# Kernel tuning notes

Hardware: AMD Instinct MI355X
Metric: run time of the kernel (lower is better)

## Reference

```python
import jax, jax.numpy as jnp
import numpy as np
import math

WS = 8
N = WS * WS
DIM = 384
HEADS = 12

def _rel_buffers():
    coords = np.stack(np.meshgrid(np.arange(WS), np.arange(WS), indexing='ij')).reshape(2, -1)
    rel = (coords[:, :, None] - coords[:, None, :]).transpose(1, 2, 0)  # [n,n,2]
    table = rel.astype(np.float32) / (WS - 1) * 8.0
    table = np.sign(table) * np.log2(np.abs(table) + 1.0) / np.log2(8.0)
    idx = rel.copy()
    idx[..., 0] += WS - 1
    idx[..., 1] += WS - 1
    idx[..., 0] *= 2 * WS - 1
    index = idx.sum(-1).astype(np.int32)  # [n,n] in [0, 225)
    return jnp.asarray(table), jnp.asarray(index)

def setup_inputs() -> dict:
    key = jax.random.key(0)
    ks = jax.random.split(key, 9)
    b_ = 4096
    nW = 1024
    table, index = _rel_buffers()
    return {
        'x': jax.random.normal(ks[0], (b_, N, DIM), jnp.float32),
        'mask': jax.random.normal(ks[1], (nW, N, N), jnp.float32),
        'qkv_w': jax.random.normal(ks[2], (DIM, 3 * DIM), jnp.float32) * 0.02,
        'qkv_b': jax.random.normal(ks[3], (3 * DIM,), jnp.float32) * 0.02,
        'proj_w': jax.random.normal(ks[4], (DIM, DIM), jnp.float32) * 0.02,
        'proj_b': jax.random.normal(ks[5], (DIM,), jnp.float32) * 0.02,
        'logit_scale': jnp.full((HEADS, 1, 1), math.log(10.0), jnp.float32),
        'cpb_w1': jax.random.normal(ks[6], (2, 512), jnp.float32) * 0.5,
        'cpb_b1': jax.random.normal(ks[7], (512,), jnp.float32) * 0.02,
        'cpb_w2': jax.random.normal(ks[8], (512, HEADS), jnp.float32) * 0.05,
        'rel_coords_table': table,
        'rel_pos_index': index,
    }

def _l2norm(t):
    # torch F.normalize: x / max(||x||, eps)
    return t / jnp.maximum(jnp.linalg.norm(t, axis=-1, keepdims=True), 1e-12)

def reference(x, mask, qkv_w, qkv_b, proj_w, proj_b, logit_scale, cpb_w1, cpb_b1, cpb_w2, rel_coords_table, rel_pos_index):
    b_, n, c = x.shape
    h = HEADS
    d = c // h
    qkv = (x @ qkv_w + qkv_b).reshape(b_, n, 3, h, d).transpose(2, 0, 3, 1, 4)
    q, k, v = qkv[0], qkv[1], qkv[2]  # [b,h,n,d]
    q = _l2norm(q)
    k = _l2norm(k)
    scale = jnp.exp(jnp.minimum(logit_scale, math.log(100.0)))  # [h,1,1]
    attn = jnp.einsum('bhqd,bhkd->bhqk', q, k) * scale[None]
    # continuous position bias MLP + gather
    bias_tab = jax.nn.relu(rel_coords_table @ cpb_w1 + cpb_b1) @ cpb_w2  # [n,n,h]
    bias = bias_tab.reshape(-1, h)[rel_pos_index.reshape(-1)].reshape(n, n, h)
    bias = 16.0 * jax.nn.sigmoid(bias.transpose(2, 0, 1))  # [h,n,n]
    attn = attn + bias[None]
    nW = mask.shape[0]
    attn = attn.reshape(b_ // nW, nW, h, n, n) + mask[None, :, None]
    attn = attn.reshape(b_, h, n, n)
    attn = jax.nn.softmax(attn, axis=-1)
    out = jnp.einsum('bhqk,bhkd->bqhd', attn, v).reshape(b_, n, c)
    return out @ proj_w + proj_b
```

## Files before the change

kernel.cpp:

```cpp
#include <hip/hip_runtime.h>
#include <hip/hip_fp16.h>

typedef _Float16 f16;
typedef _Float16 f16x8 __attribute__((ext_vector_type(8)));
typedef _Float16 f16x4 __attribute__((ext_vector_type(4)));
typedef float f32x4 __attribute__((ext_vector_type(4)));

#define NH 12
#define NWIN 4096

__device__ __forceinline__ void gload16(const void* g, void* l) {
  __builtin_amdgcn_global_load_lds(
      (const __attribute__((address_space(1))) void*)g,
      (__attribute__((address_space(3))) void*)l, 16, 0, 0);
}


__global__ __launch_bounds__(256) void k_cvt_x(const float* __restrict__ in,
                                               f16* __restrict__ out, long n4) {
  long i = (long)blockIdx.x * 256 + threadIdx.x;
  long stride = (long)gridDim.x * 256;
  for (; i < n4; i += stride) {
    float4 v = ((const float4*)in)[i];
    f16x4 o = {(f16)v.x, (f16)v.y, (f16)v.z, (f16)v.w};
    ((f16x4*)out)[i] = o;
  }
}

__global__ __launch_bounds__(256) void k_transpose(const float* __restrict__ in,
                                                   f16* __restrict__ out, int K, int N) {
  long i = (long)blockIdx.x * 256 + threadIdx.x;
  if (i >= (long)K * N) return;
  int n = (int)(i / K);
  int k = (int)(i - (long)n * K);
  out[i] = (f16)in[(long)k * N + n];
}

__global__ __launch_bounds__(64) void k_cpb(const float* __restrict__ table,
                                            const int* __restrict__ ridx,
                                            const float* __restrict__ w1,
                                            const float* __restrict__ b1,
                                            const float* __restrict__ w2,
                                            float* __restrict__ biasout) {
  int p = blockIdx.x * 64 + threadIdx.x;
  int idx = ridx[p];
  float t0 = table[idx * 2], t1 = table[idx * 2 + 1];
  float acc[NH] = {};
  for (int u = 0; u < 512; u++) {
    float hv = fmaxf(t0 * w1[u] + t1 * w1[512 + u] + b1[u], 0.f);
#pragma unroll
    for (int h = 0; h < NH; h++) acc[h] += hv * w2[u * NH + h];
  }
  for (int h = 0; h < NH; h++) biasout[h * 4096 + p] = 16.f / (1.f + __expf(-acc[h]));
}

template <int MODE, int NXB>
__global__ __launch_bounds__(256) void k_gemm(const f16* __restrict__ A,
                                              const f16* __restrict__ Bt,
                                              const float* __restrict__ bias,
                                              void* __restrict__ out, int K) {
  __shared__ f16 As[128 * 32];
  __shared__ f16 Bs[128 * 32];
  const int lin = blockIdx.x;
  const int idx = lin % (NXB * 8);
  const int xn = idx >> 3;
  const int ym = (lin / (NXB * 8)) * 8 + (idx & 7);
  const int tid = threadIdx.x;
  const int lane = tid & 63, wid = tid >> 6;
  const int wm = wid & 1, wn = wid >> 1;

  f32x4 acc[4][4] = {};
  const long arow = (long)ym * 128;
  const long brow = (long)xn * 128;

  for (int kk = 0; kk < K; kk += 32) {
    __syncthreads();
#pragma unroll
    for (int j = 0; j < 2; j++) {
      int r = wid * 32 + j * 16 + (lane >> 2);
      int co = kk + (lane & 3) * 8;
      gload16(A + (arow + r) * K + co, As + (wid * 32 + j * 16) * 32);
      gload16(Bt + (brow + r) * K + co, Bs + (wid * 32 + j * 16) * 32);
    }
    __syncthreads();
    f16x8 am[4], bn[4];
#pragma unroll
    for (int t = 0; t < 4; t++) {
      am[t] = *(const f16x8*)&As[(wm * 64 + t * 16 + (lane & 15)) * 32 + (lane >> 4) * 8];
      bn[t] = *(const f16x8*)&Bs[(wn * 64 + t * 16 + (lane & 15)) * 32 + (lane >> 4) * 8];
    }
#pragma unroll
    for (int mt = 0; mt < 4; mt++)
#pragma unroll
      for (int nt = 0; nt < 4; nt++)
        acc[mt][nt] = __builtin_amdgcn_mfma_f32_16x16x32_f16(am[mt], bn[nt], acc[mt][nt], 0, 0, 0);
  }

  const int quad = lane >> 4, col0 = lane & 15;
#pragma unroll
  for (int mt = 0; mt < 4; mt++) {
#pragma unroll
    for (int nt = 0; nt < 4; nt++) {
      int c = xn * 128 + wn * 64 + nt * 16 + col0;
      float bc = bias[c];
#pragma unroll
      for (int reg = 0; reg < 4; reg++) {
        long m = arow + wm * 64 + mt * 16 + quad * 4 + reg;
        float v = acc[mt][nt][reg] + bc;
        if (MODE == 0) {
          int which = c / 384;
          int rem = c - which * 384;
          int hh = rem >> 5, d = rem & 31;
          long b = m >> 6;
          long n = m & 63;
          ((f16*)out)[(((long)which * (NWIN * NH) + b * NH + hh) * 64 + n) * 32 + d] = (f16)v;
        } else {
          ((float*)out)[m * 384 + c] = v;
        }
      }
    }
  }
}

__global__ __launch_bounds__(256) void k_attn(const f16* __restrict__ qkv,
                                              const float* __restrict__ mask,
                                              const float* __restrict__ bias,
                                              const float* __restrict__ lsc,
                                              f16* __restrict__ aout) {
  __shared__ f16 qs[64 * 32];
  __shared__ f16 ks[64 * 32];
  __shared__ f16 vt[32 * 72];
  __shared__ float sm[64 * 64];
  __shared__ f16 ps[64 * 72];

  const int bh = blockIdx.x;
  const int b = bh / NH;
  const int h = bh - b * NH;
  const int w = b & 1023;
  const int tid = threadIdx.x;
  const int lane = tid & 63, wid = tid >> 6;

  const long HB = (long)NWIN * NH * 64 * 32;
  const f16* qg = qkv + (long)bh * 2048;

  f16x8 qv = ((const f16x8*)qg)[tid];
  f16x8 kv = ((const f16x8*)(qg + HB))[tid];
  f16x8 vv = ((const f16x8*)(qg + 2 * HB))[tid];

  float ssq = 0.f, ssk = 0.f;
#pragma unroll
  for (int j = 0; j < 8; j++) {
    float xq = (float)qv[j]; ssq += xq * xq;
    float xk = (float)kv[j]; ssk += xk * xk;
  }
  ssq += __shfl_xor(ssq, 1); ssq += __shfl_xor(ssq, 2);
  ssk += __shfl_xor(ssk, 1); ssk += __shfl_xor(ssk, 2);
  float lscale = __expf(fminf(lsc[h], 4.6051701860f));
  float qsc = lscale / fmaxf(sqrtf(ssq), 1e-12f);
  float ksc = 1.f / fmaxf(sqrtf(ssk), 1e-12f);

  f16x8 qn, kn;
#pragma unroll
  for (int j = 0; j < 8; j++) {
    qn[j] = (f16)((float)qv[j] * qsc);
    kn[j] = (f16)((float)kv[j] * ksc);
  }
  ((f16x8*)qs)[tid] = qn;
  ((f16x8*)ks)[tid] = kn;
  {
    int vrow = tid >> 2, d0 = (tid & 3) * 8;
#pragma unroll
    for (int j = 0; j < 8; j++) vt[(d0 + j) * 72 + vrow] = vv[j];
  }
  {
    const float4* bp = (const float4*)(bias + (long)h * 4096);
    const float4* mp = (const float4*)(mask + (long)w * 4096);
#pragma unroll
    for (int j = 0; j < 4; j++) {
      int i4 = tid + 256 * j;
      float4 bb = bp[i4];
      float4 mm = mp[i4];
      bb.x += mm.x; bb.y += mm.y; bb.z += mm.z; bb.w += mm.w;
      ((float4*)sm)[i4] = bb;
    }
  }
  __syncthreads();

  const int col0 = lane & 15, quad = lane >> 4;
  f16x8 aq = *(const f16x8*)&qs[(wid * 16 + col0) * 32 + quad * 8];
  f32x4 s[4];
#pragma unroll
  for (int nt = 0; nt < 4; nt++) {
    f16x8 bk = *(const f16x8*)&ks[(nt * 16 + col0) * 32 + quad * 8];
    f32x4 z = {};
    s[nt] = __builtin_amdgcn_mfma_f32_16x16x32_f16(aq, bk, z, 0, 0, 0);
  }

  float rinv[4];
#pragma unroll
  for (int reg = 0; reg < 4; reg++) {
    int r = wid * 16 + quad * 4 + reg;
    float m_ = -1e30f;
#pragma unroll
    for (int nt = 0; nt < 4; nt++) {
      s[nt][reg] += sm[r * 64 + nt * 16 + col0];
      m_ = fmaxf(m_, s[nt][reg]);
    }
    m_ = fmaxf(m_, __shfl_xor(m_, 1));
    m_ = fmaxf(m_, __shfl_xor(m_, 2));
    m_ = fmaxf(m_, __shfl_xor(m_, 4));
    m_ = fmaxf(m_, __shfl_xor(m_, 8));
    float l_ = 0.f;
#pragma unroll
    for (int nt = 0; nt < 4; nt++) {
      float p = __expf(s[nt][reg] - m_);
      s[nt][reg] = p;
      l_ += p;
    }
    l_ += __shfl_xor(l_, 1);
    l_ += __shfl_xor(l_, 2);
    l_ += __shfl_xor(l_, 4);
    l_ += __shfl_xor(l_, 8);
    rinv[reg] = 1.f / l_;
#pragma unroll
    for (int nt = 0; nt < 4; nt++) ps[r * 72 + nt * 16 + col0] = (f16)s[nt][reg];
  }
  __syncthreads();

  f32x4 o[2] = {};
#pragma unroll
  for (int kkk = 0; kkk < 2; kkk++) {
    f16x8 ap = *(const f16x8*)&ps[(wid * 16 + col0) * 72 + kkk * 32 + quad * 8];
#pragma unroll
    for (int nt = 0; nt < 2; nt++) {
      f16x8 bv = *(const f16x8*)&vt[(nt * 16 + col0) * 72 + kkk * 32 + quad * 8];
      o[nt] = __builtin_amdgcn_mfma_f32_16x16x32_f16(ap, bv, o[nt], 0, 0, 0);
    }
  }
#pragma unroll
  for (int nt = 0; nt < 2; nt++)
#pragma unroll
    for (int reg = 0; reg < 4; reg++) {
      int r = wid * 16 + quad * 4 + reg;
      int d = nt * 16 + col0;
      float v = o[nt][reg] * rinv[reg];
      aout[((long)b * 64 + r) * 384 + h * 32 + d] = (f16)v;
    }
}


extern "C" void kernel_launch(void* const* d_in, const int* in_sizes, int n_in,
                              void* d_out, int out_size, void* d_ws, size_t ws_size,
                              hipStream_t stream) {
  const float* x      = (const float*)d_in[0];
  const float* mask   = (const float*)d_in[1];
  const float* qkv_w  = (const float*)d_in[2];
  const float* qkv_b  = (const float*)d_in[3];
  const float* proj_w = (const float*)d_in[4];
  const float* proj_b = (const float*)d_in[5];
  const float* lsc    = (const float*)d_in[6];
  const float* cpb_w1 = (const float*)d_in[7];
  const float* cpb_b1 = (const float*)d_in[8];
  const float* cpb_w2 = (const float*)d_in[9];
  const float* table  = (const float*)d_in[10];
  const int* ridx     = (const int*)d_in[11];
  float* out = (float*)d_out;

  char* ws = (char*)d_ws;
  const long NQKV = (long)3 * NWIN * NH * 64 * 32;
  f16* qkvbuf = (f16*)ws;
  f16* xh     = (f16*)(ws + NQKV * 2);
  f16* aoutbuf = xh;
  f16* wtq    = (f16*)(ws + NQKV * 2 + 201326592L);
  f16* wtp    = (f16*)(ws + NQKV * 2 + 201326592L + 884736L);
  float* biasbuf = (float*)(ws + NQKV * 2 + 201326592L + 884736L + 294912L);

  k_cvt_x<<<4096, 256, 0, stream>>>(x, xh, 100663296L / 4);
  k_transpose<<<(1152 * 384) / 256, 256, 0, stream>>>(qkv_w, wtq, 384, 1152);
  k_transpose<<<(384 * 384) / 256, 256, 0, stream>>>(proj_w, wtp, 384, 384);
  k_cpb<<<64, 64, 0, stream>>>(table, ridx, cpb_w1, cpb_b1, cpb_w2, biasbuf);

  k_gemm<0, 9><<<2048 * 9, 256, 0, stream>>>(xh, wtq, qkv_b, qkvbuf, 384);

  k_attn<<<NWIN * NH, 256, 0, stream>>>(qkvbuf, mask, biasbuf, lsc, aoutbuf);

  k_gemm<1, 3><<<2048 * 3, 256, 0, stream>>>(aoutbuf, wtp, proj_b, out, 384);
}
```

Baseline: 1.536 ms.

## Make GEMM persistent with double-buffered LDS prefetch across tiles

Turns the GEMM kernel into a persistent one. Each block now walks a run of consecutive output tiles (24 for QKV, 8 for projection) on a fixed grid of 768 blocks. Shared memory is double-buffered so the next K-slice, or the first slice of the next tile, is fetched with global_load_lds while the current slice feeds the MFMAs. This cuts one barrier per K step and hides load latency. In exchange the grouped-M swizzle used for L2 reuse is dropped in favour of row-major tile order, and the larger LDS footprint plus the 3-blocks-per-SM launch bound may constrain occupancy.

```diff
diff --git a/kernel.cpp b/kernel.cpp
--- a/kernel.cpp
+++ b/kernel.cpp
@@ -54,68 +54,104 @@
   for (int h = 0; h < NH; h++) biasout[h * 4096 + p] = 16.f / (1.f + __expf(-acc[h]));
 }
 
-template <int MODE, int NXB>
-__global__ __launch_bounds__(256) void k_gemm(const f16* __restrict__ A,
-                                              const f16* __restrict__ Bt,
-                                              const float* __restrict__ bias,
-                                              void* __restrict__ out, int K) {
-  __shared__ f16 As[128 * 32];
-  __shared__ f16 Bs[128 * 32];
-  const int lin = blockIdx.x;
-  const int idx = lin % (NXB * 8);
-  const int xn = idx >> 3;
-  const int ym = (lin / (NXB * 8)) * 8 + (idx & 7);
+template <int MODE, int NXB, int TPB>
+__global__ __launch_bounds__(256, 3) void k_gemm(const f16* __restrict__ A,
+                                                 const f16* __restrict__ Bt,
+                                                 const float* __restrict__ bias,
+                                                 void* __restrict__ out, int K) {
+  __shared__ f16 smem[2 * 8192];
   const int tid = threadIdx.x;
   const int lane = tid & 63, wid = tid >> 6;
   const int wm = wid & 1, wn = wid >> 1;
+  const int quad = lane >> 4, col0 = lane & 15;
+
+  const int r0 = wid * 32 + (lane >> 2);
+  const int co0 = (lane & 3) * 8;
+  const int ldsoff = (wid * 32) * 32;
+
+  const int lin0 = blockIdx.x * TPB;
+
+  auto rows_of = [&](int t, long& ar, long& br) {
+    int lin = lin0 + t;
+    int ym = lin / NXB;
+    int xn = lin - ym * NXB;
+    ar = (long)ym * 128;
+    br = (long)xn * 128;
+  };
+
+  auto stage = [&](int buf, long ar, long br, int kk) {
+#pragma unroll
+    for (int j = 0; j < 2; j++) {
+      gload16(A + (ar + r0 + j * 16) * K + co0 + kk,
+              smem + buf * 8192 + ldsoff + j * 16 * 32);
+      gload16(Bt + (br + r0 + j * 16) * K + co0 + kk,
+              smem + buf * 8192 + 4096 + ldsoff + j * 16 * 32);
+    }
+  };
 
   f32x4 acc[4][4] = {};
-  const long arow = (long)ym * 128;
-  const long brow = (long)xn * 128;
-
-  for (int kk = 0; kk < K; kk += 32) {
-    __syncthreads();
-#pragma unroll
-    for (int j = 0; j < 2; j++) {
-      int r = wid * 32 + j * 16 + (lane >> 2);
-      int co = kk + (lane & 3) * 8;
-      gload16(A + (arow + r) * K + co, As + (wid * 32 + j * 16) * 32);
-      gload16(Bt + (brow + r) * K + co, Bs + (wid * 32 + j * 16) * 32);
-    }
-    __syncthreads();
-    f16x8 am[4], bn[4];
-#pragma unroll
-    for (int t = 0; t < 4; t++) {
-      am[t] = *(const f16x8*)&As[(wm * 64 + t * 16 + (lane & 15)) * 32 + (lane >> 4) * 8];
-      bn[t] = *(const f16x8*)&Bs[(wn * 64 + t * 16 + (lane & 15)) * 32 + (lane >> 4) * 8];
-    }
-#pragma unroll
-    for (int mt = 0; mt < 4; mt++)
-#pragma unroll
-      for (int nt = 0; nt < 4; nt++)
-        acc[mt][nt] = __builtin_amdgcn_mfma_f32_16x16x32_f16(am[mt], bn[nt], acc[mt][nt], 0, 0, 0);
-  }
-
-  const int quad = lane >> 4, col0 = lane & 15;
-#pragma unroll
-  for (int mt = 0; mt < 4; mt++) {
-#pragma unroll
-    for (int nt = 0; nt < 4; nt++) {
-      int c = xn * 128 + wn * 64 + nt * 16 + col0;
-      float bc = bias[c];
-#pragma unroll
-      for (int reg = 0; reg < 4; reg++) {
-        long m = arow + wm * 64 + mt * 16 + quad * 4 + reg;
-        float v = acc[mt][nt][reg] + bc;
-        if (MODE == 0) {
-          int which = c / 384;
-          int rem = c - which * 384;
-          int hh = rem >> 5, d = rem & 31;
-          long b = m >> 6;
-          long n = m & 63;
-          ((f16*)out)[(((long)which * (NWIN * NH) + b * NH + hh) * 64 + n) * 32 + d] = (f16)v;
-        } else {
-          ((float*)out)[m * 384 + c] = v;
+  long ar, br;
+  rows_of(0, ar, br);
+  stage(0, ar, br, 0);
+  __syncthreads();
+  int cur = 0;
+
+#pragma unroll 1
+  for (int t = 0; t < TPB; t++) {
+    rows_of(t, ar, br);
+#pragma unroll 1
+    for (int kk = 0; kk < K; kk += 32) {
+      if (kk + 32 < K) {
+        stage(cur ^ 1, ar, br, kk + 32);
+      } else if (t + 1 < TPB) {
+        long a2, b2;
+        rows_of(t + 1, a2, b2);
+        stage(cur ^ 1, a2, b2, 0);
+      }
+      const f16* As = smem + cur * 8192;
+      const f16* Bs = As + 4096;
+      f16x8 am[4], bn[4];
+#pragma unroll
+      for (int tt = 0; tt < 4; tt++) {
+        am[tt] = *(const f16x8*)&As[(wm * 64 + tt * 16 + col0) * 32 + quad * 8];
+        bn[tt] = *(const f16x8*)&Bs[(wn * 64 + tt * 16 + col0) * 32 + quad * 8];
+      }
+#pragma unroll
+      for (int mt = 0; mt < 4; mt++)
+#pragma unroll
+        for (int nt = 0; nt < 4; nt++)
+          acc[mt][nt] = __builtin_amdgcn_mfma_f32_16x16x32_f16(am[mt], bn[nt], acc[mt][nt], 0, 0, 0);
+      __syncthreads();
+      cur ^= 1;
+    }
+
+    {
+      int lin = lin0 + t;
+      int ym = lin / NXB;
+      int xn = lin - ym * NXB;
+      const long arow = (long)ym * 128;
+#pragma unroll
+      for (int mt = 0; mt < 4; mt++) {
+#pragma unroll
+        for (int nt = 0; nt < 4; nt++) {
+          int c = xn * 128 + wn * 64 + nt * 16 + col0;
+          float bc = bias[c];
+#pragma unroll
+          for (int reg = 0; reg < 4; reg++) {
+            long m = arow + wm * 64 + mt * 16 + quad * 4 + reg;
+            float v = acc[mt][nt][reg] + bc;
+            if (MODE == 0) {
+              int which = c / 384;
+              int rem = c - which * 384;
+              int hh = rem >> 5, d = rem & 31;
+              long b = m >> 6;
+              long n = m & 63;
+              ((f16*)out)[(((long)which * (NWIN * NH) + b * NH + hh) * 64 + n) * 32 + d] = (f16)v;
+            } else {
+              ((float*)out)[m * 384 + c] = v;
+            }
+          }
+          acc[mt][nt] = (f32x4){0.f, 0.f, 0.f, 0.f};
         }
       }
     }
@@ -280,9 +316,9 @@
   k_transpose<<<(384 * 384) / 256, 256, 0, stream>>>(proj_w, wtp, 384, 384);
   k_cpb<<<64, 64, 0, stream>>>(table, ridx, cpb_w1, cpb_b1, cpb_w2, biasbuf);
 
-  k_gemm<0, 9><<<2048 * 9, 256, 0, stream>>>(xh, wtq, qkv_b, qkvbuf, 384);
+  k_gemm<0, 9, 24><<<768, 256, 0, stream>>>(xh, wtq, qkv_b, qkvbuf, 384);
 
   k_attn<<<NWIN * NH, 256, 0, stream>>>(qkvbuf, mask, biasbuf, lsc, aoutbuf);
 
-  k_gemm<1, 3><<<2048 * 3, 256, 0, stream>>>(aoutbuf, wtp, proj_b, out, 384);
-}
+  k_gemm<1, 3, 8><<<768, 256, 0, stream>>>(aoutbuf, wtp, proj_b, out, 384);
+}
```

Result: slower. 1.591 ms (+3.6%).
